# Kernel tuning notes

Hardware: AMD Instinct MI355X
Metric: run time of the kernel (lower is better)

Reference implementation:

```python
import jax, jax.numpy as jnp
import numpy as np

L, B, E, H, HID = 2048, 4, 512, 8, 2048
HD = E // H


def setup_inputs() -> dict:
    key = jax.random.key(0)
    ks = jax.random.split(key, 6)
    s = 0.02
    x = jax.random.normal(ks[0], (L, B, E), jnp.float32)
    in_proj_w = jax.random.normal(ks[1], (3 * E, E), jnp.float32) * s
    in_proj_b = jnp.zeros((3 * E,), jnp.float32)
    out_w = jax.random.normal(ks[2], (E, E), jnp.float32) * s
    out_b = jnp.zeros((E,), jnp.float32)
    w1 = jax.random.normal(ks[3], (HID, E), jnp.float32) * s  # torch Linear: (out, in)
    b1 = jnp.zeros((HID,), jnp.float32)
    w2 = jax.random.normal(ks[4], (E, HID), jnp.float32) * s
    b2 = jnp.zeros((E,), jnp.float32)
    ln_g = jnp.ones((E,), jnp.float32)
    ln_b = jnp.zeros((E,), jnp.float32)
    return {"x": x, "in_proj_w": in_proj_w, "in_proj_b": in_proj_b,
            "out_w": out_w, "out_b": out_b, "w1": w1, "b1": b1,
            "w2": w2, "b2": b2, "ln_g": ln_g, "ln_b": ln_b}


def _pos_encoding(S, Emb, dtype):
    # even i: sin((t+1) * 10000^(-i/E)); odd i: cos((t+1) * 10000^(-(i+1)/E))
    t = jnp.arange(S, dtype=dtype)[:, None]
    i = jnp.arange(Emb, dtype=dtype)[None, :]
    even = jnp.sin((t + 1.0) * jnp.power(10000.0, -i / Emb))
    odd = jnp.cos((t + 1.0) * jnp.power(10000.0, -(i + 1.0) / Emb))
    return jnp.where(jnp.arange(Emb)[None, :] % 2 == 0, even, odd)  # (S, Emb)


def _layernorm(x, g, b, eps=1e-5):
    mu = jnp.mean(x, axis=-1, keepdims=True)
    var = jnp.mean(jnp.square(x - mu), axis=-1, keepdims=True)
    return (x - mu) * jax.lax.rsqrt(var + eps) * g + b


def _mha(x, in_proj_w, in_proj_b, out_w, out_b):
    # x: (L, B, E); self-attention, torch MultiheadAttention semantics
    qkv = jnp.einsum('lbe,fe->lbf', x, in_proj_w) + in_proj_b
    q, k, v = jnp.split(qkv, 3, axis=-1)
    q = q.reshape(L, B, H, HD)
    k = k.reshape(L, B, H, HD)
    v = v.reshape(L, B, H, HD)
    scores = jnp.einsum('lbhd,mbhd->bhlm', q, k) / np.sqrt(HD).astype(np.float32)
    attn = jax.nn.softmax(scores, axis=-1)
    o = jnp.einsum('bhlm,mbhd->lbhd', attn, v).reshape(L, B, E)
    return jnp.einsum('lbe,fe->lbf', o, out_w) + out_b


def reference(x, in_proj_w, in_proj_b, out_w, out_b, w1, b1, w2, b2, ln_g, ln_b):
    # positional encoding: varies along dim1, broadcasts along dim0 (as in source)
    pe = _pos_encoding(x.shape[1], x.shape[2], x.dtype)  # (B, E)
    x = x + pe[None, :, :]
    # Post-Norm path
    x = _layernorm(_mha(x, in_proj_w, in_proj_b, out_w, out_b) + x, ln_g, ln_b)
    h = jax.nn.gelu(jnp.einsum('lbe,he->lbh', x, w1) + b1, approximate=False)
    ff = jnp.einsum('lbh,eh->lbe', h, w2) + b2
    x = _layernorm(ff + x, ln_g, ln_b)
    return x
```

## Files before the change

### kernel.cpp

```cpp
#include <hip/hip_runtime.h>

typedef unsigned short u16;
typedef unsigned int   u32;
typedef u16  u16x2 __attribute__((ext_vector_type(2)));
typedef u16  u16x4 __attribute__((ext_vector_type(4)));
typedef u16  u16x8 __attribute__((ext_vector_type(8)));
typedef short s8v  __attribute__((ext_vector_type(8)));
typedef short s4v  __attribute__((ext_vector_type(4)));
typedef float f4v  __attribute__((ext_vector_type(4)));
typedef u32  u32x2 __attribute__((ext_vector_type(2)));

#define L_SEQ 2048
#define B_SZ  4
#define E_DIM 512
#define H_CNT 8
#define HD    64
#define HID   2048
#define M_ROWS (L_SEQ * B_SZ)
#define QSCALE 0.18033688011112042f

__device__ __forceinline__ u16 f2b(float f) {
    unsigned u = __builtin_bit_cast(unsigned, f);
    u += 0x7fffu + ((u >> 16) & 1u);
    return (u16)(u >> 16);
}
__device__ __forceinline__ float b2f(u16 u) {
    u32 x = ((u32)u) << 16; return __builtin_bit_cast(float, x);
}
#if defined(__has_builtin)
#if __has_builtin(__builtin_amdgcn_cvt_pk_bf16_f32)
#define HAVE_PK_BF16 1
#endif
#endif
__device__ __forceinline__ u32 pk_trunc(float a, float b) {
#ifdef HAVE_PK_BF16
    typedef __bf16 bf2 __attribute__((ext_vector_type(2)));
    bf2 r = __builtin_amdgcn_cvt_pk_bf16_f32(a, b);
    return __builtin_bit_cast(u32, r);
#else
    u32 ua = __builtin_bit_cast(u32, a), ub = __builtin_bit_cast(u32, b);
    return (ua >> 16) | (ub & 0xffff0000u);
#endif
}
__device__ __forceinline__ void gload_lds16(const u16* g, u16* l) {
    __builtin_amdgcn_global_load_lds((__attribute__((address_space(1))) void*)(u16*)g,
                                     (__attribute__((address_space(3))) void*)l, 16, 0, 0);
}
__device__ __forceinline__ float gelu_f(float v) {
    float y2 = v * (1.5957691216f + 0.0713548576f * v * v);
    return v / (1.0f + __expf(-y2));
}

__global__ __launch_bounds__(256) void pe_tab_k(float* __restrict__ pet) {
    int i = blockIdx.x * 256 + threadIdx.x;
    int e = i & (E_DIM - 1);
    float t = (float)(i >> 9) + 1.0f;
    int ee = (e & 1) ? (e + 1) : e;
    float w = exp2f((-(float)ee / 512.0f) * 13.287712379549449f);
    pet[i] = (e & 1) ? cosf(t * w) : sinf(t * w);
}

__global__ __launch_bounds__(256) void pe_add_k(const float* __restrict__ x,
                                                const float* __restrict__ pet,
                                                u16* __restrict__ xpb) {
    int idx = (blockIdx.x * 256 + threadIdx.x) * 4;
    f4v v = *(const f4v*)(x + idx);
    f4v p = *(const f4v*)(pet + (idx & 2047));
    u16x4 o;
#pragma unroll
    for (int i = 0; i < 4; ++i) o[i] = f2b(v[i] + p[i]);
    *(u16x4*)(xpb + idx) = o;
}

__global__ __launch_bounds__(256) void conv4_k(const float* __restrict__ s1, u16* __restrict__ d1, int n1,
                                               const float* __restrict__ s2, u16* __restrict__ d2, int n2,
                                               const float* __restrict__ s3, u16* __restrict__ d3, int n3,
                                               const float* __restrict__ s4, u16* __restrict__ d4) {
    int o = (blockIdx.x * 256 + threadIdx.x) * 4;
    const float* s; u16* d;
    if (o < n1) { s = s1; d = d1; }
    else { o -= n1;
        if (o < n2) { s = s2; d = d2; }
        else { o -= n2;
            if (o < n3) { s = s3; d = d3; }
            else { o -= n3; s = s4; d = d4; } } }
    f4v v = *(const f4v*)(s + o);
    u16x4 q;
#pragma unroll
    for (int i = 0; i < 4; ++i) q[i] = f2b(v[i]);
    *(u16x4*)(d + o) = q;
}

template <int NP, bool WRITEF, bool WRITEB>
__global__ __launch_bounds__(256)
void ln_c(const u16* __restrict__ p0, const u16* __restrict__ p1,
          const u16* __restrict__ p2, const u16* __restrict__ p3,
          const float* __restrict__ bias, const u16* __restrict__ resid,
          const float* __restrict__ gw, const float* __restrict__ bw,
          float* __restrict__ outF, u16* __restrict__ outB) {
    int wave = threadIdx.x >> 6, lane = threadIdx.x & 63;
    size_t row = (size_t)blockIdx.x * 4 + wave;
    size_t off = row * E_DIM + lane * 8;
    u16x8 rv = *(const u16x8*)(resid + off);
    f4v a, b;
#pragma unroll
    for (int i = 0; i < 4; ++i) { a[i] = b2f(rv[i]); b[i] = b2f(rv[i + 4]); }
    a += *(const f4v*)(bias + lane * 8);
    b += *(const f4v*)(bias + lane * 8 + 4);
    const u16* ps[4] = {p0, p1, p2, p3};
#pragma unroll
    for (int z = 0; z < NP; ++z) {
        u16x8 t = *(const u16x8*)(ps[z] + off);
#pragma unroll
        for (int i = 0; i < 4; ++i) { a[i] += b2f(t[i]); b[i] += b2f(t[i + 4]); }
    }
    float s = (a[0] + a[1]) + (a[2] + a[3]) + (b[0] + b[1]) + (b[2] + b[3]);
#pragma unroll
    for (int o = 1; o < 64; o <<= 1) s += __shfl_xor(s, o, 64);
    float mu = s * (1.0f / E_DIM);
    float q = 0.f;
#pragma unroll
    for (int i = 0; i < 4; ++i) { float d = a[i] - mu; q += d * d; }
#pragma unroll
    for (int i = 0; i < 4; ++i) { float d = b[i] - mu; q += d * d; }
#pragma unroll
    for (int o = 1; o < 64; o <<= 1) q += __shfl_xor(q, o, 64);
    float rstd = rsqrtf(q * (1.0f / E_DIM) + 1e-5f);
    f4v g0 = *(const f4v*)(gw + lane * 8), g1 = *(const f4v*)(gw + lane * 8 + 4);
    f4v w0 = *(const f4v*)(bw + lane * 8), w1 = *(const f4v*)(bw + lane * 8 + 4);
    f4v y0, y1;
#pragma unroll
    for (int i = 0; i < 4; ++i) { y0[i] = (a[i] - mu) * rstd * g0[i] + w0[i];
                                  y1[i] = (b[i] - mu) * rstd * g1[i] + w1[i]; }
    if (WRITEF) {
        *(f4v*)(outF + off)     = y0;
        *(f4v*)(outF + off + 4) = y1;
    }
    if (WRITEB) {
        u16x8 o;
#pragma unroll
        for (int i = 0; i < 4; ++i) { o[i] = f2b(y0[i]); o[i + 4] = f2b(y1[i]); }
        *(u16x8*)(outB + off) = o;
    }
}

__global__ __launch_bounds__(256) void transpose_v_k(const u16* __restrict__ vb,
                                                     u16* __restrict__ vt) {
    __shared__ __align__(16) u16 T[64 * 66];
    int t = threadIdx.x;
    int lt = blockIdx.x, bh = blockIdx.y;
    const u16* src = vb + (size_t)bh * (L_SEQ * HD) + (size_t)lt * 64 * HD;
    int lr = t >> 2, d0 = (t & 3) * 16;
    s8v va = *(const s8v*)(src + lr * HD + d0);
    s8v vb8 = *(const s8v*)(src + lr * HD + d0 + 8);
#pragma unroll
    for (int c = 0; c < 4; ++c) {
        u16x2 p0; p0[0] = (u16)va[c * 2]; p0[1] = (u16)va[c * 2 + 1];
        u16x2 p1; p1[0] = (u16)vb8[c * 2]; p1[1] = (u16)vb8[c * 2 + 1];
        *(u16x2*)(&T[lr * 66 + d0 + c * 2])     = p0;
        *(u16x2*)(&T[lr * 66 + d0 + 8 + c * 2]) = p1;
    }
    __syncthreads();
    int d = t >> 2, l0 = (t & 3) * 16;
    u16 tmp[16];
#pragma unroll
    for (int i = 0; i < 16; ++i) tmp[i] = T[(l0 + i) * 66 + d];
    u16* dst = vt + (size_t)bh * (L_SEQ * HD) + (size_t)d * L_SEQ + lt * 64 + l0;
    u16x8 o0, o1;
#pragma unroll
    for (int i = 0; i < 8; ++i) { o0[i] = tmp[i]; o1[i] = tmp[8 + i]; }
    *(u16x8*)dst       = o0;
    *(u16x8*)(dst + 8) = o1;
}

template <int MODE, int NT>
__global__ __launch_bounds__(256, 4)
void gemm_bt(const u16* __restrict__ A, const u16* __restrict__ Bw,
             const float* __restrict__ bias, int M, int N, int K,
             u16* __restrict__ outB,
             u16* __restrict__ oq, u16* __restrict__ okk, u16* __restrict__ ov) {
    __shared__ __align__(16) u16 As[2][128 * 32];
    __shared__ __align__(16) u16 Bs[2][128 * 32];
    const int tid = threadIdx.x;
    const int wave = tid >> 6, lane = tid & 63;
    const int col = lane & 15, quad = lane >> 4;
    const int n = blockIdx.x;
    const int xcd = n & 7, loc = n >> 3;
    const int mpx = (M / 128) >> 3;
    const int bm = (xcd * mpx + loc / NT) * 128;
    const int bn = (loc % NT) * 128;
    const int wm = (wave >> 1) * 64, wn = (wave & 1) * 64;
    f4v acc[4][4] = {};
    const int srow = wave * 16 + (lane >> 2);
    const int soff = (lane & 3) * 8;
    const u16* Ag = A + (size_t)(bm + srow) * K + soff;
    const u16* Bg = Bw + (size_t)(bn + srow) * K + soff;
    const int wo = wave * 512;
    gload_lds16(Ag,                  &As[0][wo]);
    gload_lds16(Ag + (size_t)64 * K, &As[0][wo + 2048]);
    gload_lds16(Bg,                  &Bs[0][wo]);
    gload_lds16(Bg + (size_t)64 * K, &Bs[0][wo + 2048]);
    const int nit = K >> 5;
    for (int t = 0; t < nit; ++t) {
        const int cur = t & 1, nxt = cur ^ 1;
        __syncthreads();
        if (t + 1 < nit) {
            const int kc = (t + 1) * 32;
            gload_lds16(Ag + kc,                  &As[nxt][wo]);
            gload_lds16(Ag + (size_t)64 * K + kc, &As[nxt][wo + 2048]);
            gload_lds16(Bg + kc,                  &Bs[nxt][wo]);
            gload_lds16(Bg + (size_t)64 * K + kc, &Bs[nxt][wo + 2048]);
        }
        s8v af[4], bf[4];
#pragma unroll
        for (int i = 0; i < 4; ++i) af[i] = *(const s8v*)(&As[cur][(wm + i * 16 + col) * 32 + quad * 8]);
#pragma unroll
        for (int j = 0; j < 4; ++j) bf[j] = *(const s8v*)(&Bs[cur][(wn + j * 16 + col) * 32 + quad * 8]);
#pragma unroll
        for (int i = 0; i < 4; ++i)
#pragma unroll
            for (int j = 0; j < 4; ++j)
                acc[i][j] = __builtin_amdgcn_mfma_f32_16x16x32_bf16(af[i], bf[j], acc[i][j], 0, 0, 0);
    }
#pragma unroll
    for (int j = 0; j < 4; ++j) {
        int gn = bn + wn + j * 16 + col;
        float bv = bias[gn];
        int which = gn >> 9, hh = (gn >> 6) & 7, d = gn & 63;
        u16* dst = (MODE == 0) ? ((which == 0) ? oq : ((which == 1) ? okk : ov)) : outB;
        float qs = (MODE == 0 && which == 0) ? QSCALE : 1.0f;
#pragma unroll
        for (int i = 0; i < 4; ++i) {
            int gm0 = bm + wm + i * 16 + quad * 4;
#pragma unroll
            for (int r = 0; r < 4; ++r) {
                float v = acc[i][j][r] + bv;
                int m = gm0 + r;
                if (MODE == 2) {
                    outB[(size_t)m * N + gn] = f2b(gelu_f(v));
                } else {
                    int l = m >> 2, bb = m & 3;
                    dst[((size_t)(bb * H_CNT + hh) * L_SEQ + l) * HD + d] = f2b(v * qs);
                }
            }
        }
    }
}

__global__ __launch_bounds__(256, 4)
void gemm_ks(const u16* __restrict__ A, const u16* __restrict__ Bw,
             int N, int K, int Kper,
             u16* __restrict__ q0, u16* __restrict__ q1) {
    __shared__ __align__(16) u16 As[2][128 * 32];
    __shared__ __align__(16) u16 Bs[2][128 * 32];
    const int tid = threadIdx.x;
    const int wave = tid >> 6, lane = tid & 63;
    const int col = lane & 15, quad = lane >> 4;
    const int n = blockIdx.x;
    const int xcd = n & 7, loc = n >> 3;
    const int bn = (loc & 3) * 128;
    const int bm = (xcd * 8 + ((loc >> 2) & 7)) * 128;
    const int kz = loc >> 5;
    u16* pz = kz ? q1 : q0;
    const int wm = (wave >> 1) * 64, wn = (wave & 1) * 64;
    f4v acc[4][4] = {};
    const int srow = wave * 16 + (lane >> 2);
    const int soff = (lane & 3) * 8;
    const u16* Ag = A + (size_t)(bm + srow) * K + kz * Kper + soff;
    const u16* Bg = Bw + (size_t)(bn + srow) * K + kz * Kper + soff;
    const int wo = wave * 512;
    gload_lds16(Ag,                  &As[0][wo]);
    gload_lds16(Ag + (size_t)64 * K, &As[0][wo + 2048]);
    gload_lds16(Bg,                  &Bs[0][wo]);
    gload_lds16(Bg + (size_t)64 * K, &Bs[0][wo + 2048]);
    const int nit = Kper >> 5;
    for (int t = 0; t < nit; ++t) {
        const int cur = t & 1, nxt = cur ^ 1;
        __syncthreads();
        if (t + 1 < nit) {
            const int kc = (t + 1) * 32;
            gload_lds16(Ag + kc,                  &As[nxt][wo]);
            gload_lds16(Ag + (size_t)64 * K + kc, &As[nxt][wo + 2048]);
            gload_lds16(Bg + kc,                  &Bs[nxt][wo]);
            gload_lds16(Bg + (size_t)64 * K + kc, &Bs[nxt][wo + 2048]);
        }
        s8v af[4], bf[4];
#pragma unroll
        for (int i = 0; i < 4; ++i) af[i] = *(const s8v*)(&As[cur][(wm + i * 16 + col) * 32 + quad * 8]);
#pragma unroll
        for (int j = 0; j < 4; ++j) bf[j] = *(const s8v*)(&Bs[cur][(wn + j * 16 + col) * 32 + quad * 8]);
#pragma unroll
        for (int i = 0; i < 4; ++i)
#pragma unroll
            for (int j = 0; j < 4; ++j)
                acc[i][j] = __builtin_amdgcn_mfma_f32_16x16x32_bf16(af[i], bf[j], acc[i][j], 0, 0, 0);
    }
#pragma unroll
    for (int j = 0; j < 4; ++j) {
        int gn = bn + wn + j * 16 + col;
#pragma unroll
        for (int i = 0; i < 4; ++i) {
            int m0 = bm + wm + i * 16 + quad * 4;
#pragma unroll
            for (int r = 0; r < 4; ++r)
                pz[(size_t)(m0 + r) * N + gn] = f2b(acc[i][j][r]);
        }
    }
}

__global__ __launch_bounds__(256, 4)
void attn_k(const u16* __restrict__ qg, const u16* __restrict__ kg,
            const u16* __restrict__ vtg,
            u16* __restrict__ po0, u16* __restrict__ po1,
            u16* __restrict__ po2, u16* __restrict__ po3, float* __restrict__ lbuf) {
    __shared__ __align__(16) u16 Ks[2][2][64 * 32];
    __shared__ __align__(16) u16 Vs[2][2][64 * 32];
    const int tid = threadIdx.x;
    const int wave = tid >> 6, lane = tid & 63;
    const int col = lane & 15, quad = lane >> 4;
    const int qc = blockIdx.x, kz = blockIdx.y, bh = blockIdx.z;
    const size_t base = (size_t)bh * (L_SEQ * HD);
    s8v qf[2][2];
#pragma unroll
    for (int t = 0; t < 2; ++t) {
        const int qrow = qc * 128 + wave * 32 + t * 16 + col;
#pragma unroll
        for (int hh = 0; hh < 2; ++hh)
            qf[t][hh] = *(const s8v*)(qg + base + (size_t)qrow * HD + hh * 32 + quad * 8);
    }
    f4v oa[2][4] = {};
    f4v la[2] = {};
    const s4v vones = {0x3F80, 0x3F80, 0x3F80, 0x3F80};
    const int h = wave & 1, r0 = (wave >> 1) * 16;
    const int srow = lane >> 2, c = lane & 3;
    const int cp = c ^ ((srow >> 1) & 3);
    const u16* Kg = kg + base + (size_t)(r0 + srow) * HD + h * 32 + cp * 8;
    const u16* Vg = vtg + base + (size_t)(r0 + srow) * L_SEQ + h * 32 + cp * 8;
    const int kt0 = kz * 8;
    {
        const int kv0 = kt0 * 64;
        gload_lds16(Kg + (size_t)kv0 * HD,        &Ks[0][h][r0 * 32]);
        gload_lds16(Kg + (size_t)(kv0 + 32) * HD, &Ks[0][h][(r0 + 32) * 32]);
        gload_lds16(Vg + kv0,                     &Vs[0][h][r0 * 32]);
        gload_lds16(Vg + kv0 + (size_t)32 * L_SEQ,&Vs[0][h][(r0 + 32) * 32]);
    }
    const int perm = (col >> 1) & 3;
#pragma unroll
    for (int it = 0; it < 8; ++it) {
        const int cur = it & 1, nxt = cur ^ 1;
        __syncthreads();
        if (it + 1 < 8) {
            const int kv0 = (kt0 + it + 1) * 64;
            gload_lds16(Kg + (size_t)kv0 * HD,        &Ks[nxt][h][r0 * 32]);
            gload_lds16(Kg + (size_t)(kv0 + 32) * HD, &Ks[nxt][h][(r0 + 32) * 32]);
            gload_lds16(Vg + kv0,                     &Vs[nxt][h][r0 * 32]);
            gload_lds16(Vg + kv0 + (size_t)32 * L_SEQ,&Vs[nxt][h][(r0 + 32) * 32]);
        }
        f4v st[2][4];
#pragma unroll
        for (int j = 0; j < 4; ++j) {
            s8v k0 = *(const s8v*)(&Ks[cur][0][(j * 16 + col) * 32 + ((quad ^ perm) * 8)]);
            s8v k1 = *(const s8v*)(&Ks[cur][1][(j * 16 + col) * 32 + ((quad ^ perm) * 8)]);
#pragma unroll
            for (int t = 0; t < 2; ++t) {
                f4v z = {};
                z = __builtin_amdgcn_mfma_f32_16x16x32_bf16(k0, qf[t][0], z, 0, 0, 0);
                z = __builtin_amdgcn_mfma_f32_16x16x32_bf16(k1, qf[t][1], z, 0, 0, 0);
                st[t][j] = z;
            }
        }
        s4v pt[2][4];
#pragma unroll
        for (int t = 0; t < 2; ++t)
#pragma unroll
            for (int j = 0; j < 4; ++j) {
                f4v p;
#pragma unroll
                for (int r = 0; r < 4; ++r) p[r] = exp2f(st[t][j][r]);
                u32x2 pk;
                pk[0] = pk_trunc(p[0], p[1]);
                pk[1] = pk_trunc(p[2], p[3]);
                pt[t][j] = __builtin_bit_cast(s4v, pk);
            }
#pragma unroll
        for (int cc = 0; cc < 4; ++cc) {
            const int hh = cc >> 1;
            const int ch8 = (cc & 1) * 2 + (quad >> 1);
#pragma unroll
            for (int dj = 0; dj < 4; ++dj) {
                s4v vf = *(const s4v*)(&Vs[cur][hh][(dj * 16 + col) * 32 + ((ch8 ^ perm) * 8) + (quad & 1) * 4]);
#pragma unroll
                for (int t = 0; t < 2; ++t)
                    oa[t][dj] = __builtin_amdgcn_mfma_f32_16x16x16bf16_1k(pt[t][cc], vf, oa[t][dj], 0, 0, 0);
            }
#pragma unroll
            for (int t = 0; t < 2; ++t)
                la[t] = __builtin_amdgcn_mfma_f32_16x16x16bf16_1k(pt[t][cc], vones, la[t], 0, 0, 0);
        }
    }
    if (col == 0) {
#pragma unroll
        for (int t = 0; t < 2; ++t)
#pragma unroll
            for (int r = 0; r < 4; ++r)
                lbuf[kz * 65536 + bh * 2048 + (qc * 128 + wave * 32 + t * 16 + quad * 4 + r)] = la[t][r];
    }
    u16* pg = (kz == 0) ? po0 : (kz == 1) ? po1 : (kz == 2) ? po2 : po3;
    const int b = bh >> 3, hd = bh & 7;
#pragma unroll
    for (int t = 0; t < 2; ++t)
#pragma unroll
        for (int r = 0; r < 4; ++r) {
            int lrow = qc * 128 + wave * 32 + t * 16 + quad * 4 + r;
            size_t mrow = (size_t)(lrow * 4 + b) * E_DIM + hd * HD;
#pragma unroll
            for (int dj = 0; dj < 4; ++dj)
                pg[mrow + dj * 16 + col] = f2b(oa[t][dj][r]);
        }
}

__global__ __launch_bounds__(256)
void combine_k(const u16* __restrict__ p0, const u16* __restrict__ p1,
               const u16* __restrict__ p2, const u16* __restrict__ p3,
               const float* __restrict__ lbuf, u16* __restrict__ out) {
    int idx8 = blockIdx.x * 256 + threadIdx.x;
    int m = idx8 >> 6;
    int e0 = (idx8 & 63) * 8;
    int b = m & 3, lrow = m >> 2, h = e0 >> 6;
    int li = (b * 8 + h) * 2048 + lrow;
    float inv = 1.0f / (lbuf[li] + lbuf[65536 + li] + lbuf[131072 + li] + lbuf[196608 + li]);
    size_t off = (size_t)m * E_DIM + e0;
    u16x8 a0 = *(const u16x8*)(p0 + off);
    u16x8 a1 = *(const u16x8*)(p1 + off);
    u16x8 a2 = *(const u16x8*)(p2 + off);
    u16x8 a3 = *(const u16x8*)(p3 + off);
    u16x8 o;
#pragma unroll
    for (int i = 0; i < 8; ++i)
        o[i] = f2b(((b2f(a0[i]) + b2f(a1[i])) + (b2f(a2[i]) + b2f(a3[i]))) * inv);
    *(u16x8*)(out + off) = o;
}

extern "C" void kernel_launch(void* const* d_in, const int* in_sizes, int n_in,
                              void* d_out, int out_size, void* d_ws, size_t ws_size,
                              hipStream_t stream) {
    const float* x     = (const float*)d_in[0];
    const float* w_qkv = (const float*)d_in[1];
    const float* b_qkv = (const float*)d_in[2];
    const float* w_out = (const float*)d_in[3];
    const float* b_out = (const float*)d_in[4];
    const float* w1    = (const float*)d_in[5];
    const float* b1    = (const float*)d_in[6];
    const float* w2    = (const float*)d_in[7];
    const float* b2    = (const float*)d_in[8];
    const float* ln_g  = (const float*)d_in[9];
    const float* ln_b  = (const float*)d_in[10];

    char* ws = (char*)d_ws;
    u16*   WQKV = (u16*)(ws + 0);
    u16*   WOUT = (u16*)(ws + 1572864);
    u16*   W1B  = (u16*)(ws + 2097152);
    u16*   W2B  = (u16*)(ws + 4194304);
    u16*   XPB  = (u16*)(ws + 6291456);
    u16*   QB   = (u16*)(ws + 14680064);
    u16*   KB   = (u16*)(ws + 23068672);
    u16*   VB   = (u16*)(ws + 31457280);
    u16*   VT   = (u16*)(ws + 39845888);
    u16*   AP0  = (u16*)(ws + 48234496);
    u16*   AP1  = (u16*)(ws + 56623104);
    u16*   AP2  = (u16*)(ws + 65011712);
    u16*   AP3  = (u16*)(ws + 73400320);
    float* LB   = (float*)(ws + 81788928);
    float* PET  = (float*)(ws + 82837504);
    u16*   OB   = VB;
    u16*   OP0  = (u16*)(ws + 48234496);
    u16*   OP1  = (u16*)(ws + 56623104);
    u16*   X3B  = QB;
    u16*   HB   = (u16*)(ws + 48234496);
    u16*   FP0  = XPB;
    u16*   FP1  = KB;

    pe_tab_k<<<8, 256, 0, stream>>>(PET);
    pe_add_k<<<4096, 256, 0, stream>>>(x, PET, XPB);
    conv4_k<<<3072, 256, 0, stream>>>(w_qkv, WQKV, 3 * E_DIM * E_DIM,
                                      w_out, WOUT, E_DIM * E_DIM,
                                      w1, W1B, HID * E_DIM,
                                      w2, W2B);
    gemm_bt<0, 12><<<768, 256, 0, stream>>>(XPB, WQKV, b_qkv, M_ROWS, 3 * E_DIM, E_DIM,
                                            nullptr, QB, KB, VB);
    transpose_v_k<<<dim3(32, 32), 256, 0, stream>>>(VB, VT);
    attn_k<<<dim3(16, 4, 32), 256, 0, stream>>>(QB, KB, VT, AP0, AP1, AP2, AP3, LB);
    combine_k<<<2048, 256, 0, stream>>>(AP0, AP1, AP2, AP3, LB, OB);
    gemm_ks<<<512, 256, 0, stream>>>(OB, WOUT, E_DIM, E_DIM, 256, OP0, OP1);
    ln_c<2, false, true><<<2048, 256, 0, stream>>>(OP0, OP1, nullptr, nullptr,
                                                   b_out, XPB, ln_g, ln_b, nullptr, X3B);
    gemm_bt<2, 16><<<1024, 256, 0, stream>>>(X3B, W1B, b1, M_ROWS, HID, E_DIM,
                                             HB, nullptr, nullptr, nullptr);
    gemm_ks<<<512, 256, 0, stream>>>(HB, W2B, E_DIM, HID, 1024, FP0, FP1);
    ln_c<2, true, false><<<2048, 256, 0, stream>>>(FP0, FP1, nullptr, nullptr,
                                                   b2, X3B, ln_g, ln_b, (float*)d_out, nullptr);
}
```

Baseline: 268.2 us.

## Use 16x16x32 MFMA for PV product by permuting K rows in LDS

Replaces the 16x16x16 bf16 MFMAs in the P·V and row-sum accumulation with 16x16x32 MFMAs, halving the instruction count for that stage. To make the S-tile output layout line up with the wider K-dimension operand, the K rows are loaded into LDS in a permuted order so adjacent score tiles pack into 8-element operands without shuffles. It also swaps exp2f for the raw hardware exp2 builtin. The row permutation must exactly match the MFMA register layout, otherwise results become wrong.

After: 258.2 us. 1.04x faster.

```diff
diff --git a/kernel.cpp b/kernel.cpp
--- a/kernel.cpp
+++ b/kernel.cpp
@@ -9,6 +9,7 @@
 typedef short s4v  __attribute__((ext_vector_type(4)));
 typedef float f4v  __attribute__((ext_vector_type(4)));
 typedef u32  u32x2 __attribute__((ext_vector_type(2)));
+typedef u32  u32x4 __attribute__((ext_vector_type(4)));
 
 #define L_SEQ 2048
 #define B_SZ  4
@@ -330,19 +331,20 @@
     }
     f4v oa[2][4] = {};
     f4v la[2] = {};
-    const s4v vones = {0x3F80, 0x3F80, 0x3F80, 0x3F80};
+    const s8v vones8 = {0x3F80, 0x3F80, 0x3F80, 0x3F80, 0x3F80, 0x3F80, 0x3F80, 0x3F80};
     const int h = wave & 1, r0 = (wave >> 1) * 16;
     const int srow = lane >> 2, c = lane & 3;
     const int cp = c ^ ((srow >> 1) & 3);
-    const u16* Kg = kg + base + (size_t)(r0 + srow) * HD + h * 32 + cp * 8;
+    const int sig = ((srow >> 2) << 3) + ((r0 >> 4) << 2) + (srow & 3);
+    const u16* Kg = kg + base + (size_t)sig * HD + h * 32 + cp * 8;
     const u16* Vg = vtg + base + (size_t)(r0 + srow) * L_SEQ + h * 32 + cp * 8;
     const int kt0 = kz * 8;
     {
         const int kv0 = kt0 * 64;
-        gload_lds16(Kg + (size_t)kv0 * HD,        &Ks[0][h][r0 * 32]);
-        gload_lds16(Kg + (size_t)(kv0 + 32) * HD, &Ks[0][h][(r0 + 32) * 32]);
-        gload_lds16(Vg + kv0,                     &Vs[0][h][r0 * 32]);
-        gload_lds16(Vg + kv0 + (size_t)32 * L_SEQ,&Vs[0][h][(r0 + 32) * 32]);
+        gload_lds16(Kg + (size_t)kv0 * HD,         &Ks[0][h][r0 * 32]);
+        gload_lds16(Kg + (size_t)(kv0 + 32) * HD,  &Ks[0][h][(r0 + 32) * 32]);
+        gload_lds16(Vg + kv0,                      &Vs[0][h][r0 * 32]);
+        gload_lds16(Vg + kv0 + (size_t)32 * L_SEQ, &Vs[0][h][(r0 + 32) * 32]);
     }
     const int perm = (col >> 1) & 3;
 #pragma unroll
@@ -351,10 +353,10 @@
         __syncthreads();
         if (it + 1 < 8) {
             const int kv0 = (kt0 + it + 1) * 64;
-            gload_lds16(Kg + (size_t)kv0 * HD,        &Ks[nxt][h][r0 * 32]);
-            gload_lds16(Kg + (size_t)(kv0 + 32) * HD, &Ks[nxt][h][(r0 + 32) * 32]);
-            gload_lds16(Vg + kv0,                     &Vs[nxt][h][r0 * 32]);
-            gload_lds16(Vg + kv0 + (size_t)32 * L_SEQ,&Vs[nxt][h][(r0 + 32) * 32]);
+            gload_lds16(Kg + (size_t)kv0 * HD,         &Ks[nxt][h][r0 * 32]);
+            gload_lds16(Kg + (size_t)(kv0 + 32) * HD,  &Ks[nxt][h][(r0 + 32) * 32]);
+            gload_lds16(Vg + kv0,                      &Vs[nxt][h][r0 * 32]);
+            gload_lds16(Vg + kv0 + (size_t)32 * L_SEQ, &Vs[nxt][h][(r0 + 32) * 32]);
         }
         f4v st[2][4];
 #pragma unroll
@@ -369,33 +371,36 @@
                 st[t][j] = z;
             }
         }
-        s4v pt[2][4];
+        u32 pk[2][4][2];
 #pragma unroll
         for (int t = 0; t < 2; ++t)
 #pragma unroll
             for (int j = 0; j < 4; ++j) {
                 f4v p;
 #pragma unroll
-                for (int r = 0; r < 4; ++r) p[r] = exp2f(st[t][j][r]);
-                u32x2 pk;
-                pk[0] = pk_trunc(p[0], p[1]);
-                pk[1] = pk_trunc(p[2], p[3]);
-                pt[t][j] = __builtin_bit_cast(s4v, pk);
+                for (int r = 0; r < 4; ++r) p[r] = __builtin_amdgcn_exp2f(st[t][j][r]);
+                pk[t][j][0] = pk_trunc(p[0], p[1]);
+                pk[t][j][1] = pk_trunc(p[2], p[3]);
             }
 #pragma unroll
-        for (int cc = 0; cc < 4; ++cc) {
-            const int hh = cc >> 1;
-            const int ch8 = (cc & 1) * 2 + (quad >> 1);
+        for (int c2 = 0; c2 < 2; ++c2) {
+            s8v pf[2];
+#pragma unroll
+            for (int t = 0; t < 2; ++t) {
+                u32x4 q4 = {pk[t][2 * c2][0], pk[t][2 * c2][1],
+                            pk[t][2 * c2 + 1][0], pk[t][2 * c2 + 1][1]};
+                pf[t] = __builtin_bit_cast(s8v, q4);
+            }
 #pragma unroll
             for (int dj = 0; dj < 4; ++dj) {
-                s4v vf = *(const s4v*)(&Vs[cur][hh][(dj * 16 + col) * 32 + ((ch8 ^ perm) * 8) + (quad & 1) * 4]);
+                s8v vf = *(const s8v*)(&Vs[cur][c2][(dj * 16 + col) * 32 + ((quad ^ perm) * 8)]);
 #pragma unroll
                 for (int t = 0; t < 2; ++t)
-                    oa[t][dj] = __builtin_amdgcn_mfma_f32_16x16x16bf16_1k(pt[t][cc], vf, oa[t][dj], 0, 0, 0);
+                    oa[t][dj] = __builtin_amdgcn_mfma_f32_16x16x32_bf16(pf[t], vf, oa[t][dj], 0, 0, 0);
             }
 #pragma unroll
             for (int t = 0; t < 2; ++t)
-                la[t] = __builtin_amdgcn_mfma_f32_16x16x16bf16_1k(pt[t][cc], vones, la[t], 0, 0, 0);
+                la[t] = __builtin_amdgcn_mfma_f32_16x16x32_bf16(pf[t], vones8, la[t], 0, 0, 0);
         }
     }
     if (col == 0) {
```
